# Kernel optimization log

Measured on AMD Instinct MI355X. Metric: run time of the kernel, lower is better.

## Reference

```python
import jax, jax.numpy as jnp
import numpy as np
from jax import lax


def _causal_mask(shape, mask_center):
    # shape = (out_ch, in_ch, h, w); mirrors CausalConv2d mask construction
    o, i, h, w = shape
    m = np.zeros(shape, dtype=np.float32)
    m[:, :, : h // 2, :] = 1.0
    m[:, :, h // 2, : w // 2 + (0 if mask_center else 1)] = 1.0
    return jnp.asarray(m)

MASK1 = _causal_mask((16, 1, 7, 7), mask_center=True)
MASK2 = _causal_mask((16, 16, 3, 3), mask_center=False)


def _conv(x, w, b, pad):
    y = lax.conv_general_dilated(
        x, w, window_strides=(1, 1), padding=[(pad, pad), (pad, pad)],
        dimension_numbers=("NCHW", "OIHW", "NCHW"))
    return y + b[None, :, None, None]


def setup_inputs() -> dict:
    key = jax.random.key(0)
    ks = jax.random.split(key, 7)
    B, H, W = 1024, 64, 64
    x = jax.random.uniform(ks[0], (B, 1, H, W), dtype=jnp.float32)
    # Kaiming-ish init scales
    w1 = jax.random.normal(ks[1], (16, 1, 7, 7), jnp.float32) * (1.0 / np.sqrt(1 * 49))
    b1 = jax.random.normal(ks[2], (16,), jnp.float32) * 0.01
    w2 = jax.random.normal(ks[3], (16, 16, 3, 3), jnp.float32) * (1.0 / np.sqrt(16 * 9))
    b2 = jax.random.normal(ks[4], (16,), jnp.float32) * 0.01
    w3 = jax.random.normal(ks[5], (1, 16, 1, 1), jnp.float32) * (1.0 / np.sqrt(16))
    b3 = jax.random.normal(ks[6], (1,), jnp.float32) * 0.01
    return {"x": x, "w1": w1, "b1": b1, "w2": w2, "b2": b2, "w3": w3, "b3": b3}


def reference(x, w1, b1, w2, b2, w3, b3):
    # PixelCNN._forward: masked conv7x7 -> relu -> masked conv3x3 -> relu -> conv1x1 -> sigmoid
    h = jax.nn.relu(_conv(x, w1 * MASK1, b1, pad=3))
    h = jax.nn.relu(_conv(h, w2 * MASK2, b2, pad=1))
    return jax.nn.sigmoid(_conv(h, w3, b3, pad=0))
```

## Files before the change

kernel.cpp:

```cpp
#include <hip/hip_runtime.h>

typedef _Float16 half8  __attribute__((ext_vector_type(8)));
typedef __fp16   fp16x2 __attribute__((ext_vector_type(2)));
typedef float    floatx4 __attribute__((ext_vector_type(4)));

#define IMG_H 64
#define IMG_W 64
#define TH 16
#define TW 32
#define INW 40
#define H1W 34
#define NH1 612
#define NPX 640
#define CP 912

__device__ __forceinline__ unsigned pk2u(float a, float b) {
    fp16x2 h = __builtin_amdgcn_cvt_pkrtz(a, b);
    return __builtin_bit_cast(unsigned, h);
}

__global__ __launch_bounds__(256, 7) void pixelcnn_mfma9(
    const float* __restrict__ x,
    const float* __restrict__ w1, const float* __restrict__ b1,
    const float* __restrict__ w2, const float* __restrict__ b2,
    const float* __restrict__ w3, const float* __restrict__ b3,
    float* __restrict__ out)
{
    __shared__ __align__(16) _Float16      s16[4 * CP];
    __shared__ __align__(16) _Float16      s_w1t[16 * 32];
    __shared__ __align__(16) unsigned char s_w2t8[16 * 96];
    __shared__ __align__(16) float         s_b1[16], s_b2[16], s_w3[16];
    __shared__ float                       s_b3;
    __shared__ __align__(16) unsigned      s_h1[2 * NPX * 2];

    const int t    = threadIdx.x;
    const int lane = t & 63;
    const int wave = t >> 6;
    const int n    = lane & 15;
    const int quad = lane >> 4;
    const int img  = blockIdx.y;
    const int btile = blockIdx.x;
    const int ty0 = (btile >> 1) * TH;
    const int tx0 = (btile & 1) * TW;

    const float* xim = x + img * (IMG_H * IMG_W);

    if (t < 210) {
        int r = t / 10, c4 = (t - r * 10) * 4;
        int gy = ty0 - 4 + r;
        int gx0 = tx0 - 4 + c4;
        float4 v  = {0.f, 0.f, 0.f, 0.f};
        float4 v2 = {0.f, 0.f, 0.f, 0.f};
        if ((unsigned)gy < IMG_H) {
            const float* rp = xim + gy * IMG_W;
            if ((unsigned)gx0 < IMG_W)       v  = *(const float4*)(rp + gx0);
            if ((unsigned)(gx0 + 4) < IMG_W) v2 = *(const float4*)(rp + gx0 + 4);
        }
        unsigned a0 = pk2u(v.x,  v.y),  a1 = pk2u(v.z,  v.w);
        unsigned a2 = pk2u(v2.x, v2.y), a3 = pk2u(v2.z, v2.w);
        unsigned m10 = (a0 >> 16) | (a1 << 16);
        unsigned m21 = (a1 >> 16) | (a2 << 16);
        unsigned m32 = (a2 >> 16) | (a3 << 16);
        int lin = r * INW + c4;
        *(uint2*)&s16[0*CP + 0 + lin + 0] = uint2{a0,  a1 };
        *(uint2*)&s16[1*CP + 3 + lin + 1] = uint2{m10, m21};
        *(uint2*)&s16[2*CP + 2 + lin + 2] = uint2{a1,  a2 };
        *(uint2*)&s16[3*CP + 1 + lin + 3] = uint2{m21, m32};
    }
    if (t < 192) {
        int c = t / 48, e = t - c * 48;
        s16[c * CP + ((4 - c) & 3) + 840 + e] = (_Float16)0.f;
    }
    {
        int ch = t >> 4, l = t & 15;
        const float* w1c = w1 + ch * 49;
#pragma unroll
        for (int j2 = 0; j2 < 2; ++j2) {
            int k = l + 16 * j2, q = k >> 3, jj = k & 7;
            float v = 0.f;
            if (q < 3)      { if (jj < 7) v = w1c[q * 7 + jj]; }
            else            { if (jj < 3) v = w1c[21 + jj];    }
            s_w1t[ch * 32 + k] = (_Float16)v;
        }
        const float* w2cl = w2 + (ch * 16 + l) * 9;
#pragma unroll
        for (int j = 0; j < 6; ++j) {
            float v = (j < 5) ? w2cl[j] : 0.f;
            unsigned q8 = (unsigned)__builtin_amdgcn_cvt_pk_fp8_f32(v, 0.f, 0, false);
            s_w2t8[ch * 96 + j * 16 + l] = (unsigned char)(q8 & 0xff);
        }
    }
    if (t < 16) { s_b1[t] = b1[t]; s_b2[t] = b2[t]; s_w3[t] = w3[t]; }
    if (t == 16) s_b3 = b3[0];
    __syncthreads();

    {
        const half8 afrag = *(const half8*)&s_w1t[n * 32 + quad * 8];
        const floatx4 bias1 = ((const floatx4*)s_b1)[quad];
        int p  = wave * 16 + n;
        int py = p / H1W, px = p - py * H1W;
        int lin1 = (py + quad) * INW + px;
        int gy = ty0 - 1 + py;
        int gx = tx0 - 1 + px;
        unsigned wd = (unsigned)((quad >> 1) * (NPX * 2) + p * 2 + (quad & 1));

#pragma unroll
        for (int i = 0; i < 10; ++i) {
            int c = px & 3;
            const _Float16* ap = &s16[c * CP + ((4 - c) & 3) + lin1];
            uint2 lo = *(const uint2*)ap;
            uint2 hi = *(const uint2*)(ap + 4);
            uint4 bu; bu.x = lo.x; bu.y = lo.y; bu.z = hi.x; bu.w = hi.y;
            half8 b = __builtin_bit_cast(half8, bu);
            floatx4 acc = bias1;
            acc = __builtin_amdgcn_mfma_f32_16x16x32_f16(afrag, b, acc, 0, 0, 0);
            bool inimg = ((unsigned)gy < IMG_H) & ((unsigned)gx < IMG_W);
            int d = __builtin_amdgcn_cvt_pk_fp8_f32(fmaxf(acc[0], 0.f), fmaxf(acc[1], 0.f), 0, false);
            d = __builtin_amdgcn_cvt_pk_fp8_f32(fmaxf(acc[2], 0.f), fmaxf(acc[3], 0.f), d, true);
            s_h1[wd] = inimg ? (unsigned)d : 0u;
            int px2 = px + 30;
            bool wrap = px2 >= H1W;
            px    = wrap ? px2 - H1W : px2;
            gy   += wrap ? 2 : 1;
            gx    = wrap ? gx - 4 : gx + 30;
            lin1 += wrap ? 76 : 70;
            wd   += 128;
        }
    }
    __syncthreads();

    {
        const long w2f0 = *(const long*)&s_w2t8[n * 96 +  0 + quad * 8];
        const long w2f1 = *(const long*)&s_w2t8[n * 96 + 32 + quad * 8];
        const long w2f2 = *(const long*)&s_w2t8[n * 96 + 64 + quad * 8];
        const floatx4 bias2 = ((const floatx4*)s_b2)[quad];
        const floatx4 w3q   = ((const floatx4*)s_w3)[quad];
        const float bias3 = s_b3;
        const int y0 = wave >> 1, x0 = (wave & 1) * 16;
        const int tqh = quad >> 1, plane = quad & 1;
        const int E0 = (y0 + 1) * H1W + x0 + n + 1;
        const char* h1b = (const char*)s_h1 + plane * (NPX * 8);
        const char* a0 = h1b + (E0 - 35 + tqh) * 8;
        const char* a1 = h1b + (E0 + (tqh ? -1 : -33)) * 8;
        const char* a2 = h1b + E0 * 8;
        float* optr = out + ((img * IMG_H) + ty0 + y0) * IMG_W + tx0 + x0 + n;

#pragma unroll
        for (int k = 0; k < 8; ++k) {
            floatx4 acc = bias2;
            acc = __builtin_amdgcn_mfma_f32_16x16x32_fp8_fp8(w2f0, *(const long*)(a0 + k * 544), acc, 0, 0, 0);
            acc = __builtin_amdgcn_mfma_f32_16x16x32_fp8_fp8(w2f1, *(const long*)(a1 + k * 544), acc, 0, 0, 0);
            acc = __builtin_amdgcn_mfma_f32_16x16x32_fp8_fp8(w2f2, *(const long*)(a2 + k * 544), acc, 0, 0, 0);
            float s = fmaxf(acc[0], 0.f) * w3q[0];
            s = fmaf(fmaxf(acc[1], 0.f), w3q[1], s);
            s = fmaf(fmaxf(acc[2], 0.f), w3q[2], s);
            s = fmaf(fmaxf(acc[3], 0.f), w3q[3], s);
            s += __shfl_xor(s, 16);
            s += __shfl_xor(s, 32);
            if (lane < 16) {
                float r = 1.f / (1.f + __expf(-(s + bias3)));
                *(float*)((char*)optr + k * 512) = r;
            }
        }
    }
}

extern "C" void kernel_launch(void* const* d_in, const int* in_sizes, int n_in,
                              void* d_out, int out_size, void* d_ws, size_t ws_size,
                              hipStream_t stream) {
    const float* x  = (const float*)d_in[0];
    const float* w1 = (const float*)d_in[1];
    const float* b1 = (const float*)d_in[2];
    const float* w2 = (const float*)d_in[3];
    const float* b2 = (const float*)d_in[4];
    const float* w3 = (const float*)d_in[5];
    const float* b3 = (const float*)d_in[6];
    float* out = (float*)d_out;

    dim3 grid(8, 1024);
    dim3 block(256);
    hipLaunchKernelGGL(pixelcnn_mfma9, grid, block, 0, stream,
                       x, w1, b1, w2, b2, w3, b3, out);
}
```

Measured before the change: 114.9 us.

## Replace three fp8 16x16x32 MFMAs with one scaled 16x16x128 MFMA

The second conv's three K=32 fp8 MFMAs per output tile become a single 16x16x128 scaled f8f6f4 MFMA with unit scales (0x7F exponent). To feed it, the h1 intermediate layout changes from two planes of 8-byte pixels to a 16-byte-per-pixel interleaved layout, and the w2 fragment is padded to 128 bytes per channel. Each lane now does two 16-byte LDS loads instead of three 8-byte loads per step. The risk is that the larger K padding adds zero work and the new layout may change LDS bank conflicts in the stage-1 writes.

Measured after the change: 115.3 us. No clear change (+0.3%).

```diff
diff --git a/kernel.cpp b/kernel.cpp
--- a/kernel.cpp
+++ b/kernel.cpp
@@ -3,6 +3,7 @@
 typedef _Float16 half8  __attribute__((ext_vector_type(8)));
 typedef __fp16   fp16x2 __attribute__((ext_vector_type(2)));
 typedef float    floatx4 __attribute__((ext_vector_type(4)));
+typedef int      intx8  __attribute__((ext_vector_type(8)));
 
 #define IMG_H 64
 #define IMG_W 64
@@ -19,7 +20,7 @@
     return __builtin_bit_cast(unsigned, h);
 }
 
-__global__ __launch_bounds__(256, 7) void pixelcnn_mfma9(
+__global__ __launch_bounds__(256, 7) void pixelcnn_mfma10(
     const float* __restrict__ x,
     const float* __restrict__ w1, const float* __restrict__ b1,
     const float* __restrict__ w2, const float* __restrict__ b2,
@@ -28,10 +29,10 @@
 {
     __shared__ __align__(16) _Float16      s16[4 * CP];
     __shared__ __align__(16) _Float16      s_w1t[16 * 32];
-    __shared__ __align__(16) unsigned char s_w2t8[16 * 96];
+    __shared__ __align__(16) unsigned char s_w2t8[16 * 128];
     __shared__ __align__(16) float         s_b1[16], s_b2[16], s_w3[16];
     __shared__ float                       s_b3;
-    __shared__ __align__(16) unsigned      s_h1[2 * NPX * 2];
+    __shared__ __align__(16) unsigned      s_h1[NPX * 4];
 
     const int t    = threadIdx.x;
     const int lane = t & 63;
@@ -84,10 +85,10 @@
         }
         const float* w2cl = w2 + (ch * 16 + l) * 9;
 #pragma unroll
-        for (int j = 0; j < 6; ++j) {
+        for (int j = 0; j < 8; ++j) {
             float v = (j < 5) ? w2cl[j] : 0.f;
             unsigned q8 = (unsigned)__builtin_amdgcn_cvt_pk_fp8_f32(v, 0.f, 0, false);
-            s_w2t8[ch * 96 + j * 16 + l] = (unsigned char)(q8 & 0xff);
+            s_w2t8[ch * 128 + j * 16 + l] = (unsigned char)(q8 & 0xff);
         }
     }
     if (t < 16) { s_b1[t] = b1[t]; s_b2[t] = b2[t]; s_w3[t] = w3[t]; }
@@ -102,7 +103,7 @@
         int lin1 = (py + quad) * INW + px;
         int gy = ty0 - 1 + py;
         int gx = tx0 - 1 + px;
-        unsigned wd = (unsigned)((quad >> 1) * (NPX * 2) + p * 2 + (quad & 1));
+        unsigned wd = (unsigned)(p * 4 + quad);
 
 #pragma unroll
         for (int i = 0; i < 10; ++i) {
@@ -124,33 +125,37 @@
             gy   += wrap ? 2 : 1;
             gx    = wrap ? gx - 4 : gx + 30;
             lin1 += wrap ? 76 : 70;
-            wd   += 128;
+            wd   += 256;
         }
     }
     __syncthreads();
 
     {
-        const long w2f0 = *(const long*)&s_w2t8[n * 96 +  0 + quad * 8];
-        const long w2f1 = *(const long*)&s_w2t8[n * 96 + 32 + quad * 8];
-        const long w2f2 = *(const long*)&s_w2t8[n * 96 + 64 + quad * 8];
+        union { uint4 u[2]; intx8 v; } aU;
+        aU.u[0] = *(const uint4*)&s_w2t8[n * 128 + quad * 32];
+        aU.u[1] = *(const uint4*)&s_w2t8[n * 128 + quad * 32 + 16];
+        const intx8 afrag2 = aU.v;
+
         const floatx4 bias2 = ((const floatx4*)s_b2)[quad];
         const floatx4 w3q   = ((const floatx4*)s_w3)[quad];
         const float bias3 = s_b3;
         const int y0 = wave >> 1, x0 = (wave & 1) * 16;
-        const int tqh = quad >> 1, plane = quad & 1;
         const int E0 = (y0 + 1) * H1W + x0 + n + 1;
-        const char* h1b = (const char*)s_h1 + plane * (NPX * 8);
-        const char* a0 = h1b + (E0 - 35 + tqh) * 8;
-        const char* a1 = h1b + (E0 + (tqh ? -1 : -33)) * 8;
-        const char* a2 = h1b + E0 * 8;
+        const int o0 = (quad == 0) ? -35 : ((quad == 1) ? -33 : 0);
+        const int o1 = (quad == 0) ? -34 : ((quad == 1) ? -1  : 0);
+        const char* p0 = (const char*)s_h1 + (E0 + o0) * 16;
+        const char* p1 = (const char*)s_h1 + (E0 + o1) * 16;
         float* optr = out + ((img * IMG_H) + ty0 + y0) * IMG_W + tx0 + x0 + n;
 
 #pragma unroll
         for (int k = 0; k < 8; ++k) {
+            union { uint4 u[2]; intx8 v; } bU;
+            bU.u[0] = *(const uint4*)(p0 + k * 1088);
+            bU.u[1] = *(const uint4*)(p1 + k * 1088);
             floatx4 acc = bias2;
-            acc = __builtin_amdgcn_mfma_f32_16x16x32_fp8_fp8(w2f0, *(const long*)(a0 + k * 544), acc, 0, 0, 0);
-            acc = __builtin_amdgcn_mfma_f32_16x16x32_fp8_fp8(w2f1, *(const long*)(a1 + k * 544), acc, 0, 0, 0);
-            acc = __builtin_amdgcn_mfma_f32_16x16x32_fp8_fp8(w2f2, *(const long*)(a2 + k * 544), acc, 0, 0, 0);
+            acc = __builtin_amdgcn_mfma_scale_f32_16x16x128_f8f6f4(
+                      afrag2, bU.v, acc, 0, 0,
+                      0, 0x7F7F7F7F, 0, 0x7F7F7F7F);
             float s = fmaxf(acc[0], 0.f) * w3q[0];
             s = fmaf(fmaxf(acc[1], 0.f), w3q[1], s);
             s = fmaf(fmaxf(acc[2], 0.f), w3q[2], s);
@@ -179,6 +184,6 @@
 
     dim3 grid(8, 1024);
     dim3 block(256);
-    hipLaunchKernelGGL(pixelcnn_mfma9, grid, block, 0, stream,
+    hipLaunchKernelGGL(pixelcnn_mfma10, grid, block, 0, stream,
                        x, w1, b1, w2, b2, w3, b3, out);
 }
```

## Load conv1 input directly from global memory, dropping the shared-memory input staging

Applied to the files above, without the earlier changes.

Removes the shared-memory staging of the fp16 input tile, with its four shifted copies. Each lane now loads its 8-float window straight from global memory (L1/L2-cached), packs it to fp16 and shifts it with 128-bit integer shifts so image borders are handled by clamped addresses. Edge tiles are handled by template specialisation on left/top position. The smaller LDS footprint lets launch bounds rise to 8 blocks per CU. The trade-off is more redundant global loads and extra ALU work per MFMA, in exchange for less LDS traffic and higher occupancy.

Measured after the change: 124.5 us. +8.3%, slower.

```diff
diff --git a/kernel.cpp b/kernel.cpp
--- a/kernel.cpp
+++ b/kernel.cpp
@@ -3,30 +3,67 @@
 typedef _Float16 half8  __attribute__((ext_vector_type(8)));
 typedef __fp16   fp16x2 __attribute__((ext_vector_type(2)));
 typedef float    floatx4 __attribute__((ext_vector_type(4)));
+typedef floatx4  floatx4a __attribute__((aligned(4)));
 
 #define IMG_H 64
 #define IMG_W 64
 #define TH 16
 #define TW 32
-#define INW 40
 #define H1W 34
 #define NH1 612
 #define NPX 640
-#define CP 912
 
 __device__ __forceinline__ unsigned pk2u(float a, float b) {
     fp16x2 h = __builtin_amdgcn_cvt_pkrtz(a, b);
     return __builtin_bit_cast(unsigned, h);
 }
 
-__global__ __launch_bounds__(256, 7) void pixelcnn_mfma9(
+template<bool LEFT, bool TOP>
+__device__ __forceinline__ void run_phase1(
+    const float* __restrict__ xim, half8 afrag, floatx4 bias1,
+    unsigned* s_h1, int px, int gy, int gx, unsigned wd, int quad)
+{
+#pragma unroll
+    for (int i = 0; i < 10; ++i) {
+        int gin = gy - 3 + quad;
+        int gc  = min(max(gin, 0), IMG_H - 1);
+        int s   = gx - 3;
+        int sc  = LEFT ? max(s, 0) : min(s, IMG_W - 8);
+        const float* rp = xim + gc * IMG_W + sc;
+        floatx4a va = *(const floatx4a*)rp;
+        floatx4a vb = *(const floatx4a*)(rp + 4);
+        unsigned long long lo = ((unsigned long long)pk2u(va[2], va[3]) << 32) | pk2u(va[0], va[1]);
+        unsigned long long hi = ((unsigned long long)pk2u(vb[2], vb[3]) << 32) | pk2u(vb[0], vb[1]);
+        __uint128_t v = ((__uint128_t)hi << 64) | lo;
+        int sh = (LEFT ? (sc - s) : (s - sc)) * 16;
+        v = LEFT ? (v << sh) : (v >> sh);
+        if (TOP) { if (gin < 0) v = 0; }
+        uint4 bu;
+        bu.x = (unsigned)v;         bu.y = (unsigned)(v >> 32);
+        bu.z = (unsigned)(v >> 64); bu.w = (unsigned)(v >> 96);
+        half8 b = __builtin_bit_cast(half8, bu);
+        floatx4 acc = bias1;
+        acc = __builtin_amdgcn_mfma_f32_16x16x32_f16(afrag, b, acc, 0, 0, 0);
+        bool inimg = ((unsigned)gy < IMG_H) & ((unsigned)gx < IMG_W);
+        int d = __builtin_amdgcn_cvt_pk_fp8_f32(fmaxf(acc[0], 0.f), fmaxf(acc[1], 0.f), 0, false);
+        d = __builtin_amdgcn_cvt_pk_fp8_f32(fmaxf(acc[2], 0.f), fmaxf(acc[3], 0.f), d, true);
+        s_h1[wd] = inimg ? (unsigned)d : 0u;
+        int px2 = px + 30;
+        bool wrap = px2 >= H1W;
+        px  = wrap ? px2 - H1W : px2;
+        gy += wrap ? 2 : 1;
+        gx  = wrap ? gx - 4 : gx + 30;
+        wd += 128;
+    }
+}
+
+__global__ __launch_bounds__(256, 8) void pixelcnn_mfma11(
     const float* __restrict__ x,
     const float* __restrict__ w1, const float* __restrict__ b1,
     const float* __restrict__ w2, const float* __restrict__ b2,
     const float* __restrict__ w3, const float* __restrict__ b3,
     float* __restrict__ out)
 {
-    __shared__ __align__(16) _Float16      s16[4 * CP];
     __shared__ __align__(16) _Float16      s_w1t[16 * 32];
     __shared__ __align__(16) unsigned char s_w2t8[16 * 96];
     __shared__ __align__(16) float         s_b1[16], s_b2[16], s_w3[16];
@@ -45,32 +82,6 @@
 
     const float* xim = x + img * (IMG_H * IMG_W);
 
-    if (t < 210) {
-        int r = t / 10, c4 = (t - r * 10) * 4;
-        int gy = ty0 - 4 + r;
-        int gx0 = tx0 - 4 + c4;
-        float4 v  = {0.f, 0.f, 0.f, 0.f};
-        float4 v2 = {0.f, 0.f, 0.f, 0.f};
-        if ((unsigned)gy < IMG_H) {
-            const float* rp = xim + gy * IMG_W;
-            if ((unsigned)gx0 < IMG_W)       v  = *(const float4*)(rp + gx0);
-            if ((unsigned)(gx0 + 4) < IMG_W) v2 = *(const float4*)(rp + gx0 + 4);
-        }
-        unsigned a0 = pk2u(v.x,  v.y),  a1 = pk2u(v.z,  v.w);
-        unsigned a2 = pk2u(v2.x, v2.y), a3 = pk2u(v2.z, v2.w);
-        unsigned m10 = (a0 >> 16) | (a1 << 16);
-        unsigned m21 = (a1 >> 16) | (a2 << 16);
-        unsigned m32 = (a2 >> 16) | (a3 << 16);
-        int lin = r * INW + c4;
-        *(uint2*)&s16[0*CP + 0 + lin + 0] = uint2{a0,  a1 };
-        *(uint2*)&s16[1*CP + 3 + lin + 1] = uint2{m10, m21};
-        *(uint2*)&s16[2*CP + 2 + lin + 2] = uint2{a1,  a2 };
-        *(uint2*)&s16[3*CP + 1 + lin + 3] = uint2{m21, m32};
-    }
-    if (t < 192) {
-        int c = t / 48, e = t - c * 48;
-        s16[c * CP + ((4 - c) & 3) + 840 + e] = (_Float16)0.f;
-    }
     {
         int ch = t >> 4, l = t & 15;
         const float* w1c = w1 + ch * 49;
@@ -99,32 +110,16 @@
         const floatx4 bias1 = ((const floatx4*)s_b1)[quad];
         int p  = wave * 16 + n;
         int py = p / H1W, px = p - py * H1W;
-        int lin1 = (py + quad) * INW + px;
         int gy = ty0 - 1 + py;
         int gx = tx0 - 1 + px;
         unsigned wd = (unsigned)((quad >> 1) * (NPX * 2) + p * 2 + (quad & 1));
 
-#pragma unroll
-        for (int i = 0; i < 10; ++i) {
-            int c = px & 3;
-            const _Float16* ap = &s16[c * CP + ((4 - c) & 3) + lin1];
-            uint2 lo = *(const uint2*)ap;
-            uint2 hi = *(const uint2*)(ap + 4);
-            uint4 bu; bu.x = lo.x; bu.y = lo.y; bu.z = hi.x; bu.w = hi.y;
-            half8 b = __builtin_bit_cast(half8, bu);
-            floatx4 acc = bias1;
-            acc = __builtin_amdgcn_mfma_f32_16x16x32_f16(afrag, b, acc, 0, 0, 0);
-            bool inimg = ((unsigned)gy < IMG_H) & ((unsigned)gx < IMG_W);
-            int d = __builtin_amdgcn_cvt_pk_fp8_f32(fmaxf(acc[0], 0.f), fmaxf(acc[1], 0.f), 0, false);
-            d = __builtin_amdgcn_cvt_pk_fp8_f32(fmaxf(acc[2], 0.f), fmaxf(acc[3], 0.f), d, true);
-            s_h1[wd] = inimg ? (unsigned)d : 0u;
-            int px2 = px + 30;
-            bool wrap = px2 >= H1W;
-            px    = wrap ? px2 - H1W : px2;
-            gy   += wrap ? 2 : 1;
-            gx    = wrap ? gx - 4 : gx + 30;
-            lin1 += wrap ? 76 : 70;
-            wd   += 128;
+        if (tx0 == 0) {
+            if (ty0 == 0) run_phase1<true,  true >(xim, afrag, bias1, s_h1, px, gy, gx, wd, quad);
+            else          run_phase1<true,  false>(xim, afrag, bias1, s_h1, px, gy, gx, wd, quad);
+        } else {
+            if (ty0 == 0) run_phase1<false, true >(xim, afrag, bias1, s_h1, px, gy, gx, wd, quad);
+            else          run_phase1<false, false>(xim, afrag, bias1, s_h1, px, gy, gx, wd, quad);
         }
     }
     __syncthreads();
@@ -179,6 +174,6 @@
 
     dim3 grid(8, 1024);
     dim3 block(256);
-    hipLaunchKernelGGL(pixelcnn_mfma9, grid, block, 0, stream,
+    hipLaunchKernelGGL(pixelcnn_mfma11, grid, block, 0, stream,
                        x, w1, b1, w2, b2, w3, b3, out);
 }
```
